# Optimization experiments

Hardware: AMD Instinct MI355X
Metric: run time of the kernel (lower is better)

Reference implementation:

```python
import jax, jax.numpy as jnp
import numpy as np

N_CLASS, N_SUPPORT, N_QUERY = 64, 5, 64
D_IN, C, WIN = 1024, 128, 5
D = C * WIN * WIN  # 3200, fine-encoder output dim


def setup_inputs() -> dict:
    key = jax.random.key(0)
    ks = jax.random.split(key, 6)
    s = 0.02  # weight init scale
    return {
        "xs": jax.random.normal(ks[0], (N_CLASS, N_SUPPORT, D_IN), jnp.float32),
        "xq": jax.random.normal(ks[1], (N_CLASS, N_QUERY, D_IN), jnp.float32),
        "W_share": jax.random.normal(ks[2], (D_IN, D), jnp.float32) * s,
        "b_share": jnp.zeros((D,), jnp.float32),
        "W_att": jax.random.normal(ks[3], (C, C), jnp.float32) * s,
        "b_att": jnp.zeros((C,), jnp.float32),
        "W_fine": jax.random.normal(ks[4], (D, D), jnp.float32) * s,
        "b_fine": jnp.zeros((D,), jnp.float32),
    }


def reference(xs, xq, W_share, b_share, W_att, b_att, W_fine, b_fine):
    n_class, n_support = xs.shape[0], xs.shape[1]
    n_query = xq.shape[1]
    ns = n_class * n_support

    # concat support + query, run shared encoder
    x = jnp.concatenate([xs.reshape(ns, -1), xq.reshape(n_class * n_query, -1)], axis=0)
    z_share = jax.nn.relu(x @ W_share + b_share)            # [N, D]
    z4 = z_share.reshape(-1, C, WIN, WIN)

    # attention head: spatial mean -> linear -> per-channel logits
    z_att = z4.mean(axis=(2, 3)) @ W_att + b_att            # [N, C]

    diag_c = jax.nn.softmax(z_att[:ns].mean(axis=0)) * C    # [C]
    w = jnp.repeat(diag_c, WIN * WIN)                       # [D] diagonal of learned metric

    # fine encoder (flatten + linear)
    z = z_share @ W_fine + b_fine                           # [N, D]
    z_proto = z[:ns].reshape(n_class, n_support, -1).mean(axis=1)  # [n_class, D]
    zq = z[ns:]                                             # [n, D]

    # attentionMetric with diagonal metric == weighted squared distance:
    # dists[i,j] = sum_d w_d (zq_i - proto_j)^2, expanded to avoid the n*m*d diff tensor
    q2 = (zq * zq) @ w                                      # [n]
    p2 = (z_proto * z_proto) @ w                            # [m]
    cross = (zq * w) @ z_proto.T                            # [n, m]
    dists = q2[:, None] + p2[None, :] - 2.0 * cross         # [n, m]

    log_p_y = jax.nn.log_softmax(-dists, axis=1).reshape(n_class, n_query, n_class)
    target = jnp.arange(n_class)
    tgt = jnp.broadcast_to(target[:, None, None], (n_class, n_query, 1))
    loss_val = -jnp.take_along_axis(log_p_y, tgt, axis=2).mean()
    y_hat = jnp.argmax(log_p_y, axis=2)
    acc_val = (y_hat == target[:, None]).astype(jnp.float32).mean()
    return loss_val, acc_val
```

## Files before the change

kernel.cpp:

```cpp
#include <hip/hip_runtime.h>
#include <math.h>

#define N_CLASS 64
#define N_SUPPORT 5
#define N_QUERY 64
#define D_IN 1024
#define C_CH 128
#define WIN 5
#define D_FEAT 3200
#define NS 320
#define NQ 4096
#define M_ROWS 4416
#define M_PAD 4480

#define ZP_SLICE  (N_CLASS * D_FEAT)
#define GT_SLICE  (128 * D_FEAT)
#define CR_SLICE  (NQ * 128)
#define NKS       10
#define LOSS_BLKS (NQ / 4)

#define PREP_X   4480
#define PREP_WS  3200
#define CONV_WF  10000

#define WS_SCALE    64.0f
#define WS_INVSCALE 0.015625f

#define WS_XF8      0u
#define WS_WSF8     4718592u
#define WS_ZSB      8126464u
#define WS_WFB      36388864u
#define WS_WFTB     56868864u
#define WS_ARENA    77348864u
#define WS_UB       98320384u
#define WS_YB       99139584u
#define WS_GT       99958784u
#define WS_WV       100777984u
#define WS_P2       100790784u
#define WS_CVEC     100791296u
#define WS_LPART    100791808u
#define WS_UPOOL    100800128u


typedef __bf16 bf16x8 __attribute__((ext_vector_type(8)));
typedef __bf16 bf16x4 __attribute__((ext_vector_type(4)));
typedef float floatx4 __attribute__((ext_vector_type(4)));
typedef __attribute__((address_space(1))) const void* gptr_t;
typedef __attribute__((address_space(3))) void* lptr_t;

__device__ __forceinline__ float waveReduceSum(float v) {
    for (int off = 32; off > 0; off >>= 1) v += __shfl_xor(v, off, 64);
    return v;
}

__global__ __launch_bounds__(256) void prep_kernel(const float* __restrict__ xs,
                                                   const float* __restrict__ xq,
                                                   const float* __restrict__ W_share,
                                                   unsigned char* __restrict__ Xf8,
                                                   unsigned char* __restrict__ Wsf8)
{
    __shared__ float tile[32][33];
    const int b = blockIdx.x;
    const int t = threadIdx.x;

    if (b < PREP_X) {
        const int e = (b * 256 + t) * 4;
        const int row = e >> 10;
        const int col = e & 1023;
        float4 v = make_float4(0.f, 0.f, 0.f, 0.f);
        if (row < NS)          v = *(const float4*)(xs + (size_t)row * D_IN + col);
        else if (row < M_ROWS) v = *(const float4*)(xq + (size_t)(row - NS) * D_IN + col);
        int p = __builtin_amdgcn_cvt_pk_fp8_f32(v.x, v.y, 0, false);
        p     = __builtin_amdgcn_cvt_pk_fp8_f32(v.z, v.w, p, true);
        const int ocol = col ^ (((row >> 1) & 1) << 3);
        *(int*)(Xf8 + (size_t)row * D_IN + ocol) = p;
        return;
    }
    const int tx = t & 31;
    const int ty = t >> 5;
    const int tb = b - PREP_X;
    const int n0 = (tb % 100) * 32;
    const int k0 = (tb / 100) * 32;
#pragma unroll
    for (int i = ty; i < 32; i += 8)
        tile[i][tx] = W_share[(size_t)(k0 + i) * D_FEAT + n0 + tx];
    __syncthreads();
#pragma unroll
    for (int i = ty; i < 32; i += 8) {
        const int p = __builtin_amdgcn_cvt_pk_fp8_f32(tile[tx][i] * WS_SCALE, 0.f,
                                                      0, false);
        const int n = n0 + i;
        const int k = (k0 + tx) ^ (((n >> 1) & 1) << 3);
        Wsf8[(size_t)n * D_IN + k] = (unsigned char)(p & 0xff);
    }
}

__global__ __launch_bounds__(256, 3) void gemm_fp8_128(const unsigned char* __restrict__ A,
                                                       const unsigned char* __restrict__ Bt,
                                                       const float* __restrict__ bias,
                                                       __bf16* __restrict__ out_bf)
{
    __shared__ __align__(16) unsigned char smem[49152];

    const int t    = threadIdx.x;
    const int lane = t & 63;
    const int w    = t >> 6;
    const int wm   = w >> 1;
    const int wn   = w & 1;

    const int bx = blockIdx.x % 25;
    const int by = blockIdx.x / 25;
    const int bm = by * 128;
    const int bn = bx * 128;

    const int q    = lane >> 4;
    const int r16  = lane & 15;
    const int m3   = (r16 >> 1) & 7;
    const int off0 = (q ^ m3) * 8;

    const int rowA = (wm * 64 + r16) * 64;
    const int rowB = (wn * 64 + r16) * 64;

    const int srow  = t >> 2;
    const int sunit = 16 * ((t & 3) ^ ((srow >> 2) & 3));

    const unsigned char* gA = A  + (size_t)(bm + srow) * D_IN + sunit;
    const unsigned char* gB = Bt + (size_t)(bn + srow) * D_IN + sunit;

    auto stage = [&](int uu, int slot) {
        const unsigned char* ga = gA + uu * 64;
        const unsigned char* gb = gB + uu * 64;
        unsigned char* l = smem + slot * 16384 + t * 16;
        __builtin_amdgcn_global_load_lds((gptr_t)ga,           (lptr_t)l,            16, 0, 0);
        __builtin_amdgcn_global_load_lds((gptr_t)(ga + 65536), (lptr_t)(l + 4096),   16, 0, 0);
        __builtin_amdgcn_global_load_lds((gptr_t)gb,           (lptr_t)(l + 8192),   16, 0, 0);
        __builtin_amdgcn_global_load_lds((gptr_t)(gb + 65536), (lptr_t)(l + 12288),  16, 0, 0);
    };

    floatx4 acc[4][4] = {};
    long av0[4], bv0[4], av1[4], bv1[4];

    auto ld16 = [&](const unsigned char* sa) {
#pragma unroll
        for (int mi = 0; mi < 4; ++mi)
            av0[mi] = *(const long*)(sa + rowA + mi * 1024 + off0);
#pragma unroll
        for (int ni = 0; ni < 4; ++ni)
            bv0[ni] = *(const long*)(sa + 8192 + rowB + ni * 1024 + off0);
#pragma unroll
        for (int mi = 0; mi < 4; ++mi)
            av1[mi] = *(const long*)(sa + rowA + mi * 1024 + (off0 ^ 32));
#pragma unroll
        for (int ni = 0; ni < 4; ++ni)
            bv1[ni] = *(const long*)(sa + 8192 + rowB + ni * 1024 + (off0 ^ 32));
    };
    auto mfma32 = [&]() {
        __builtin_amdgcn_s_setprio(1);
#pragma unroll
        for (int mi = 0; mi < 4; ++mi)
#pragma unroll
            for (int ni = 0; ni < 4; ++ni)
                acc[mi][ni] = __builtin_amdgcn_mfma_f32_16x16x32_fp8_fp8(
                    av0[mi], bv0[ni], acc[mi][ni], 0, 0, 0);
#pragma unroll
        for (int mi = 0; mi < 4; ++mi)
#pragma unroll
            for (int ni = 0; ni < 4; ++ni)
                acc[mi][ni] = __builtin_amdgcn_mfma_f32_16x16x32_fp8_fp8(
                    av1[mi], bv1[ni], acc[mi][ni], 0, 0, 0);
        __builtin_amdgcn_s_setprio(0);
    };

    stage(0, 0);
    stage(1, 1);

    for (int u = 0; u < 14; ++u) {
        const unsigned char* sa = smem + (u % 3) * 16384;
        asm volatile("s_waitcnt vmcnt(4)" ::: "memory");
        __builtin_amdgcn_s_barrier();
        ld16(sa);
        stage(u + 2, (u + 2) % 3);
        asm volatile("s_waitcnt lgkmcnt(0)" ::: "memory");
        mfma32();
    }
    {
        const unsigned char* sa = smem + (14 % 3) * 16384;
        asm volatile("s_waitcnt vmcnt(4)" ::: "memory");
        __builtin_amdgcn_s_barrier();
        ld16(sa);
        asm volatile("s_waitcnt lgkmcnt(0)" ::: "memory");
        mfma32();
    }
    {
        const unsigned char* sa = smem + (15 % 3) * 16384;
        asm volatile("s_waitcnt vmcnt(0)" ::: "memory");
        __builtin_amdgcn_s_barrier();
        ld16(sa);
        asm volatile("s_waitcnt lgkmcnt(0)" ::: "memory");
        mfma32();
    }

    __syncthreads();
    float bcol[4];
#pragma unroll
    for (int ni = 0; ni < 4; ++ni) bcol[ni] = bias[bn + wn * 64 + ni * 16 + r16];
    const int ebase = (wm * 64 + q * 4) * 256 + wn * 128 + r16 * 2;
#pragma unroll
    for (int mi = 0; mi < 4; ++mi)
#pragma unroll
        for (int ni = 0; ni < 4; ++ni) {
            const int cb = (ni ^ q) << 5;
#pragma unroll
            for (int reg = 0; reg < 4; ++reg) {
                float v = acc[mi][ni][reg] * WS_INVSCALE + bcol[ni];
                v = fmaxf(v, 0.f);
                *(__bf16*)(smem + ebase + mi * 4096 + reg * 256 + cb) = (__bf16)v;
            }
        }
    __syncthreads();
#pragma unroll
    for (int ps = 0; ps < 8; ++ps) {
        const int idx  = ps * 256 + t;
        const int row  = idx >> 4;
        const int grow = bm + row;
        if (grow < M_ROWS) {
            const int lb = row * 256 + (((idx & 15) << 4) ^ (((row >> 2) & 3) << 5));
            const int4 d = *(const int4*)(smem + lb);
            *(int4*)((char*)out_bf + ((size_t)grow * D_FEAT + bn + (idx & 15) * 8) * 2) = d;
        }
    }
}

__global__ __launch_bounds__(256) void gemm_bf16(const __bf16* __restrict__ A,
                                                 const __bf16* __restrict__ Bt,
                                                 const float* __restrict__ bias,
                                                 __bf16* __restrict__ out_bf,
                                                 float* __restrict__ out_f32,
                                                 int N, int strideK, int kIters,
                                                 int Mout, int relu, int sliceStride,
                                                 int nbx, int nby,
                                                 const float* __restrict__ attUpool,
                                                 const float* __restrict__ W_att,
                                                 const float* __restrict__ b_att,
                                                 float* __restrict__ wvec)
{
    __shared__ __align__(16) char smem[65536];
    const int t = threadIdx.x;

    if (attUpool != nullptr && blockIdx.x == gridDim.x - 1) {
        float* sW   = (float*)smem;
        float* s_pm = (float*)(smem + 16384);
        float* s_at = (float*)(smem + 16384 + 512);
        float* s_dg = (float*)(smem + 16384 + 1024);
        if (t < C_CH) {
            float a = 0.f;
            for (int p = 0; p < N_CLASS; ++p) a += attUpool[(size_t)p * C_CH + t];
            s_pm[t] = a * (1.0f / (N_CLASS * 25));
        }
        __syncthreads();
        float acc = (t < C_CH) ? b_att[t] : 0.f;
#pragma unroll
        for (int qtr = 0; qtr < 4; ++qtr) {
            const float4* src = (const float4*)(W_att + qtr * 32 * C_CH);
            float4* dst = (float4*)sW;
#pragma unroll
            for (int i = 0; i < 4; ++i) dst[i * 256 + t] = src[i * 256 + t];
            __syncthreads();
            if (t < C_CH) {
#pragma unroll
                for (int k = 0; k < 32; ++k)
                    acc += s_pm[qtr * 32 + k] * sW[k * C_CH + t];
            }
            __syncthreads();
        }
        if (t < C_CH) s_at[t] = acc;
        __syncthreads();
        if (t < C_CH) {
            float m = -INFINITY;
            for (int k = 0; k < C_CH; ++k) m = fmaxf(m, s_at[k]);
            float s = 0.f;
            for (int k = 0; k < C_CH; ++k) s += expf(s_at[k] - m);
            s_dg[t] = expf(acc - m) / s * (float)C_CH;
        }
        __syncthreads();
        for (int j = t; j < D_FEAT; j += 256) wvec[j] = s_dg[j / 25];
        return;
    }

    int bx, by, ks;
    {
        const int nbxy = nbx * nby;
        ks = blockIdx.x / nbxy;
        const int b = blockIdx.x - ks * nbxy;
        const int fg = nbx >> 3;
        const int full = fg * 8 * nby;
        if (b < full) {
            const int g = b / (8 * nby);
            const int r = b - g * 8 * nby;
            bx = g * 8 + (r & 7);
            by = r >> 3;
        } else {
            const int rem = nbx - fg * 8;
            const int r = b - full;
            bx = fg * 8 + r % rem;
            by = r / rem;
        }
    }

    const int lane = t & 63;
    const int w    = t >> 6;
    const int wm   = w >> 1;
    const int wn   = w & 1;
    const int bm   = by * 128;
    const int bn   = bx * 128;

    const int q    = lane >> 4;
    const int r16  = lane & 15;
    const int sw   = (r16 >> 1) & 3;
    const int cA   = (q ^ sw) * 8;

    const int srow   = w * 16 + (lane >> 2);
    const int sglob8 = (((lane & 3) ^ ((lane >> 3) & 3))) * 8;

    const int kBase = ks * kIters * 64;
    floatx4 acc[4][4] = {};

    auto stageb = [&](int ki, char* base) {
        const int k0 = kBase + ki * 64;
#pragma unroll
        for (int s = 0; s < 2; ++s) {
#pragma unroll
            for (int j = 0; j < 2; ++j) {
                const __bf16* ga = A  + (size_t)(bm + j * 64 + srow) * strideK
                                      + k0 + s * 32 + sglob8;
                const __bf16* gb = Bt + (size_t)(bn + j * 64 + srow) * strideK
                                      + k0 + s * 32 + sglob8;
                char* la = base +         s * 8192 + (j * 256 + w * 64) * 16;
                char* lb = base + 16384 + s * 8192 + (j * 256 + w * 64) * 16;
                __builtin_amdgcn_global_load_lds((gptr_t)ga, (lptr_t)la, 16, 0, 0);
                __builtin_amdgcn_global_load_lds((gptr_t)gb, (lptr_t)lb, 16, 0, 0);
            }
        }
    };

    stageb(0, smem);
    for (int ki = 0; ki < kIters; ++ki) {
        char* base = smem + (ki & 1) * 32768;
        __syncthreads();
        if (ki + 1 < kIters) stageb(ki + 1, smem + ((ki + 1) & 1) * 32768);

#pragma unroll
        for (int s = 0; s < 2; ++s) {
            const __bf16* sAe = (const __bf16*)(base +         s * 8192);
            const __bf16* sBe = (const __bf16*)(base + 16384 + s * 8192);
            bf16x8 av[4], bv[4];
#pragma unroll
            for (int mi = 0; mi < 4; ++mi)
                av[mi] = *(const bf16x8*)(sAe + ((wm * 64 + mi * 16 + r16) * 32 + cA));
#pragma unroll
            for (int ni = 0; ni < 4; ++ni)
                bv[ni] = *(const bf16x8*)(sBe + ((wn * 64 + ni * 16 + r16) * 32 + cA));
#pragma unroll
            for (int mi = 0; mi < 4; ++mi)
#pragma unroll
                for (int ni = 0; ni < 4; ++ni)
                    acc[mi][ni] = __builtin_amdgcn_mfma_f32_16x16x32_bf16(
                        av[mi], bv[ni], acc[mi][ni], 0, 0, 0);
        }
    }

#pragma unroll
    for (int ni = 0; ni < 4; ++ni) {
        const int col = bn + wn * 64 + ni * 16 + r16;
        const float bcol = sliceStride ? 0.f : bias[col];
#pragma unroll
        for (int mi = 0; mi < 4; ++mi) {
#pragma unroll
            for (int reg = 0; reg < 4; ++reg) {
                const int row = bm + wm * 64 + mi * 16 + q * 4 + reg;
                if (row < Mout) {
                    if (sliceStride) {
                        out_f32[(size_t)ks * sliceStride + (size_t)row * N + col] =
                            acc[mi][ni][reg];
                    } else {
                        float v = acc[mi][ni][reg] + bcol;
                        if (relu) v = fmaxf(v, 0.f);
                        if (out_f32) out_f32[(size_t)row * N + col] = v;
                        else         out_bf [(size_t)row * N + col] = (__bf16)v;
                    }
                }
            }
        }
    }
}

__global__ __launch_bounds__(256) void ut_conv_kernel(const __bf16* __restrict__ z_share,
                                                      const float* __restrict__ W_fine,
                                                      __bf16* __restrict__ u,
                                                      float* __restrict__ upool,
                                                      __bf16* __restrict__ Wfb,
                                                      __bf16* __restrict__ WfTb)
{
    __shared__ __align__(16) char smem_u[D_FEAT * 4];
    const int b = blockIdx.x;
    const int t = threadIdx.x;

    if (b >= 128) {
        float (*tile)[33] = (float(*)[33])smem_u;
        const int tb = b - 128;
        const int tx = t & 31;
        const int ty = t >> 5;
        const int n0 = (tb % 100) * 32;
        const int k0 = (tb / 100) * 32;
#pragma unroll
        for (int i = ty; i < 32; i += 8) {
            const float v = W_fine[(size_t)(k0 + i) * D_FEAT + n0 + tx];
            Wfb[(size_t)(k0 + i) * D_FEAT + n0 + tx] = (__bf16)v;
            tile[i][tx] = v;
        }
        __syncthreads();
#pragma unroll
        for (int i = ty; i < 32; i += 8)
            WfTb[(size_t)(n0 + i) * D_FEAT + k0 + tx] = (__bf16)tile[tx][i];
        return;
    }

    float* srow_ = (float*)smem_u;
    const int p = b;
    if (p >= N_CLASS) {
        for (int k = t; k < D_FEAT; k += 256) u[(size_t)p * D_FEAT + k] = (__bf16)0.f;
        return;
    }
    const __bf16* base = z_share + (size_t)(p * N_SUPPORT) * D_FEAT;
    for (int k = t; k < D_FEAT; k += 256) {
        float s = 0.f;
#pragma unroll
        for (int ss = 0; ss < N_SUPPORT; ++ss) s += (float)base[(size_t)ss * D_FEAT + k];
        s *= (1.0f / N_SUPPORT);
        u[(size_t)p * D_FEAT + k] = (__bf16)s;
        srow_[k] = s;
    }
    __syncthreads();
    if (t < C_CH) {
        float pool = 0.f;
#pragma unroll
        for (int win = 0; win < 25; ++win) pool += srow_[t * 25 + win];
        upool[(size_t)p * C_CH + t] = pool;
    }
}

__global__ __launch_bounds__(256) void y_kernel(const float* __restrict__ zp_part,
                                                const float* __restrict__ wv,
                                                const float* __restrict__ bf,
                                                __bf16* __restrict__ y,
                                                float* __restrict__ p2,
                                                float* __restrict__ cvec)
{
    __shared__ float s_red2[8];
    const int p = blockIdx.x;
    const int t = threadIdx.x;
    if (p >= N_CLASS) {
        for (int j = t; j < D_FEAT; j += 256) y[(size_t)p * D_FEAT + j] = (__bf16)0.f;
        return;
    }
    float s2 = 0.f, sc = 0.f;
    for (int j = t; j < D_FEAT; j += 256) {
        float zpf = bf[j];
#pragma unroll
        for (int ss = 0; ss < NKS; ++ss)
            zpf += zp_part[(size_t)ss * ZP_SLICE + (size_t)p * D_FEAT + j];
        const float wj = wv[j];
        y[(size_t)p * D_FEAT + j] = (__bf16)(wj * zpf);
        s2 += wj * zpf * zpf;
        sc += bf[j] * wj * zpf;
    }
    s2 = waveReduceSum(s2);
    sc = waveReduceSum(sc);
    const int lane = t & 63, wid = t >> 6;
    if (lane == 0) { s_red2[wid] = s2; s_red2[4 + wid] = sc; }
    __syncthreads();
    if (t == 0) {
        p2[p]   = s_red2[0] + s_red2[1] + s_red2[2] + s_red2[3];
        cvec[p] = s_red2[4] + s_red2[5] + s_red2[6] + s_red2[7];
    }
}

__global__ __launch_bounds__(256) void gtsum_kernel(const float* __restrict__ gp,
                                                    __bf16* __restrict__ Gt)
{
    const int i4 = blockIdx.x * 256 + threadIdx.x;
    if (i4 >= GT_SLICE / 4) return;
    float4 s = make_float4(0.f, 0.f, 0.f, 0.f);
#pragma unroll
    for (int ss = 0; ss < NKS; ++ss) {
        const float4 v = *(const float4*)(gp + (size_t)ss * GT_SLICE + i4 * 4);
        s.x += v.x; s.y += v.y; s.z += v.z; s.w += v.w;
    }
    bf16x4 o = { (__bf16)s.x, (__bf16)s.y, (__bf16)s.z, (__bf16)s.w };
    *(bf16x4*)(Gt + (size_t)i4 * 4) = o;
}

__global__ __launch_bounds__(256) void loss_kernel(const float* __restrict__ cross_part,
                                                   const float* __restrict__ p2,
                                                   const float* __restrict__ cvec,
                                                   float* __restrict__ lpart)
{
    __shared__ float s_l[4], s_a[4];
    const int t = threadIdx.x;
    const int lane = t & 63, wid = t >> 6;
    const int i = blockIdx.x * 4 + wid;
    float cr = 0.f;
#pragma unroll
    for (int ss = 0; ss < NKS; ++ss)
        cr += cross_part[(size_t)ss * CR_SLICE + (size_t)i * 128 + lane];
    const float neg = 2.0f * (cr + cvec[lane]) - p2[lane];
    float m = neg;
    for (int off = 32; off > 0; off >>= 1) m = fmaxf(m, __shfl_xor(m, off, 64));
    float e = expf(neg - m);
    float ssum = e;
    for (int off = 32; off > 0; off >>= 1) ssum += __shfl_xor(ssum, off, 64);
    const float lse = m + logf(ssum);
    const int tcls = i >> 6;
    const float negt = __shfl(neg, tcls, 64);
    float v = -neg; int bi = lane;
    for (int off = 32; off > 0; off >>= 1) {
        const float ov = __shfl_xor(v, off, 64);
        const int   oi = __shfl_xor(bi, off, 64);
        if (ov < v || (ov == v && oi < bi)) { v = ov; bi = oi; }
    }
    if (lane == 0) { s_l[wid] = lse - negt; s_a[wid] = (bi == tcls) ? 1.0f : 0.0f; }
    __syncthreads();
    if (t == 0) {
        lpart[blockIdx.x]             = s_l[0] + s_l[1] + s_l[2] + s_l[3];
        lpart[LOSS_BLKS + blockIdx.x] = s_a[0] + s_a[1] + s_a[2] + s_a[3];
    }
}

__global__ __launch_bounds__(256) void writeout_kernel(const float* __restrict__ lpart,
                                                       float* __restrict__ out)
{
    __shared__ float s_red2[8];
    const int t = threadIdx.x;
    float l = 0.f, a = 0.f;
    for (int k = t; k < LOSS_BLKS; k += 256) {
        l += lpart[k];
        a += lpart[LOSS_BLKS + k];
    }
    l = waveReduceSum(l);
    a = waveReduceSum(a);
    const int lane = t & 63, wid = t >> 6;
    if (lane == 0) { s_red2[wid] = l; s_red2[4 + wid] = a; }
    __syncthreads();
    if (t == 0) {
        out[0] = (s_red2[0] + s_red2[1] + s_red2[2] + s_red2[3]) * (1.0f / NQ);
        out[1] = (s_red2[4] + s_red2[5] + s_red2[6] + s_red2[7]) * (1.0f / NQ);
    }
}

extern "C" void kernel_launch(void* const* d_in, const int* in_sizes, int n_in,
                              void* d_out, int out_size, void* d_ws, size_t ws_size,
                              hipStream_t stream)
{
    const float* xs      = (const float*)d_in[0];
    const float* xq      = (const float*)d_in[1];
    const float* W_share = (const float*)d_in[2];
    const float* b_share = (const float*)d_in[3];
    const float* W_att   = (const float*)d_in[4];
    const float* b_att   = (const float*)d_in[5];
    const float* W_fine  = (const float*)d_in[6];
    const float* b_fine  = (const float*)d_in[7];
    float* out = (float*)d_out;

    char* ws = (char*)d_ws;
    unsigned char* Xf8  = (unsigned char*)(ws + WS_XF8);
    unsigned char* Wsf8 = (unsigned char*)(ws + WS_WSF8);
    __bf16* Zsb     = (__bf16*)(ws + WS_ZSB);
    __bf16* Wfb     = (__bf16*)(ws + WS_WFB);
    __bf16* WfTb    = (__bf16*)(ws + WS_WFTB);
    float*  arena   = (float*) (ws + WS_ARENA);
    float*  zp_part = arena;
    float*  gt_part = arena;
    float*  cr_part = arena;
    __bf16* ub      = (__bf16*)(ws + WS_UB);
    __bf16* yb      = (__bf16*)(ws + WS_YB);
    __bf16* Gt      = (__bf16*)(ws + WS_GT);
    float*  wv      = (float*) (ws + WS_WV);
    float*  p2v     = (float*) (ws + WS_P2);
    float*  cvec    = (float*) (ws + WS_CVEC);
    float*  lpart   = (float*) (ws + WS_LPART);
    float*  upool   = (float*) (ws + WS_UPOOL);

    prep_kernel<<<PREP_X + PREP_WS, 256, 0, stream>>>(xs, xq, W_share, Xf8, Wsf8);

    gemm_fp8_128<<<35 * 25, 256, 0, stream>>>(Xf8, Wsf8, b_share, Zsb);

    ut_conv_kernel<<<128 + CONV_WF, 256, 0, stream>>>(Zsb, W_fine, ub, upool,
                                                      Wfb, WfTb);

    gemm_bf16<<<25 * NKS + 1, 256, 0, stream>>>(
        ub, WfTb, nullptr, nullptr, zp_part,
        D_FEAT, D_FEAT, 5, N_CLASS, 0, ZP_SLICE, 25, 1,
        upool, W_att, b_att, wv);

    y_kernel<<<128, 256, 0, stream>>>(zp_part, wv, b_fine, yb, p2v, cvec);

    gemm_bf16<<<25 * NKS, 256, 0, stream>>>(
        yb, Wfb, nullptr, nullptr, gt_part,
        D_FEAT, D_FEAT, 5, 128, 0, GT_SLICE, 25, 1,
        nullptr, nullptr, nullptr, nullptr);

    gtsum_kernel<<<(GT_SLICE / 4 + 255) / 256, 256, 0, stream>>>(gt_part, Gt);

    gemm_bf16<<<32 * NKS, 256, 0, stream>>>(
        Zsb + (size_t)NS * D_FEAT, Gt, nullptr, nullptr, cr_part,
        128, D_FEAT, 5, NQ, 0, CR_SLICE, 1, 32,
        nullptr, nullptr, nullptr, nullptr);

    loss_kernel<<<LOSS_BLKS, 256, 0, stream>>>(cr_part, p2v, cvec, lpart);

    writeout_kernel<<<1, 256, 0, stream>>>(lpart, out);
}
```

Before: 224.6 us.

## Move W_fine bf16 convert/transpose into FP8 GEMM tail; skip unused cross columns

The W_fine to bf16 conversion and transpose work, previously extra blocks of the ut_conv kernel, now runs as a tail loop inside the FP8 shared-encoder GEMM, with each block handling 12 tiles after its epilogue. ut_kernel now only computes support means and pooling. A colLimit parameter lets the final cross GEMM skip storing columns at or beyond 64, since only 64 prototypes exist. The aim is to overlap the bandwidth-bound weight conversion with the GEMM and cut partial-sum writes, at the cost of making the GEMM blocks longer and running the conversion at the GEMM's occupancy.

```diff
diff --git a/kernel.cpp b/kernel.cpp
--- a/kernel.cpp
+++ b/kernel.cpp
@@ -98,7 +98,10 @@
 __global__ __launch_bounds__(256, 3) void gemm_fp8_128(const unsigned char* __restrict__ A,
                                                        const unsigned char* __restrict__ Bt,
                                                        const float* __restrict__ bias,
-                                                       __bf16* __restrict__ out_bf)
+                                                       __bf16* __restrict__ out_bf,
+                                                       const float* __restrict__ W_fine,
+                                                       __bf16* __restrict__ Wfb,
+                                                       __bf16* __restrict__ WfTb)
 {
     __shared__ __align__(16) unsigned char smem[49152];
 
@@ -229,6 +232,29 @@
             *(int4*)((char*)out_bf + ((size_t)grow * D_FEAT + bn + (idx & 15) * 8) * 2) = d;
         }
     }
+
+    {
+        float (*tile)[33] = (float(*)[33])smem;
+        const int tx = t & 31;
+        const int ty = t >> 5;
+        for (int it = 0; it < 12; ++it) {
+            const int tb = blockIdx.x * 12 + it;
+            if (tb >= CONV_WF) break;
+            const int n0 = (tb % 100) * 32;
+            const int k0 = (tb / 100) * 32;
+            __syncthreads();
+#pragma unroll
+            for (int i = ty; i < 32; i += 8) {
+                const float v = W_fine[(size_t)(k0 + i) * D_FEAT + n0 + tx];
+                Wfb[(size_t)(k0 + i) * D_FEAT + n0 + tx] = (__bf16)v;
+                tile[i][tx] = v;
+            }
+            __syncthreads();
+#pragma unroll
+            for (int i = ty; i < 32; i += 8)
+                WfTb[(size_t)(n0 + i) * D_FEAT + k0 + tx] = (__bf16)tile[tx][i];
+        }
+    }
 }
 
 __global__ __launch_bounds__(256) void gemm_bf16(const __bf16* __restrict__ A,
@@ -238,7 +264,7 @@
                                                  float* __restrict__ out_f32,
                                                  int N, int strideK, int kIters,
                                                  int Mout, int relu, int sliceStride,
-                                                 int nbx, int nby,
+                                                 int nbx, int nby, int colLimit,
                                                  const float* __restrict__ attUpool,
                                                  const float* __restrict__ W_att,
                                                  const float* __restrict__ b_att,
@@ -372,21 +398,23 @@
 #pragma unroll
     for (int ni = 0; ni < 4; ++ni) {
         const int col = bn + wn * 64 + ni * 16 + r16;
-        const float bcol = sliceStride ? 0.f : bias[col];
-#pragma unroll
-        for (int mi = 0; mi < 4; ++mi) {
-#pragma unroll
-            for (int reg = 0; reg < 4; ++reg) {
-                const int row = bm + wm * 64 + mi * 16 + q * 4 + reg;
-                if (row < Mout) {
-                    if (sliceStride) {
-                        out_f32[(size_t)ks * sliceStride + (size_t)row * N + col] =
-                            acc[mi][ni][reg];
-                    } else {
-                        float v = acc[mi][ni][reg] + bcol;
-                        if (relu) v = fmaxf(v, 0.f);
-                        if (out_f32) out_f32[(size_t)row * N + col] = v;
-                        else         out_bf [(size_t)row * N + col] = (__bf16)v;
+        if (col < colLimit) {
+            const float bcol = sliceStride ? 0.f : bias[col];
+#pragma unroll
+            for (int mi = 0; mi < 4; ++mi) {
+#pragma unroll
+                for (int reg = 0; reg < 4; ++reg) {
+                    const int row = bm + wm * 64 + mi * 16 + q * 4 + reg;
+                    if (row < Mout) {
+                        if (sliceStride) {
+                            out_f32[(size_t)ks * sliceStride + (size_t)row * N + col] =
+                                acc[mi][ni][reg];
+                        } else {
+                            float v = acc[mi][ni][reg] + bcol;
+                            if (relu) v = fmaxf(v, 0.f);
+                            if (out_f32) out_f32[(size_t)row * N + col] = v;
+                            else         out_bf [(size_t)row * N + col] = (__bf16)v;
+                        }
                     }
                 }
             }
@@ -394,39 +422,13 @@
     }
 }
 
-__global__ __launch_bounds__(256) void ut_conv_kernel(const __bf16* __restrict__ z_share,
-                                                      const float* __restrict__ W_fine,
-                                                      __bf16* __restrict__ u,
-                                                      float* __restrict__ upool,
-                                                      __bf16* __restrict__ Wfb,
-                                                      __bf16* __restrict__ WfTb)
-{
-    __shared__ __align__(16) char smem_u[D_FEAT * 4];
-    const int b = blockIdx.x;
+__global__ __launch_bounds__(256) void ut_kernel(const __bf16* __restrict__ z_share,
+                                                 __bf16* __restrict__ u,
+                                                 float* __restrict__ upool)
+{
+    __shared__ float srow_[D_FEAT];
+    const int p = blockIdx.x;
     const int t = threadIdx.x;
-
-    if (b >= 128) {
-        float (*tile)[33] = (float(*)[33])smem_u;
-        const int tb = b - 128;
-        const int tx = t & 31;
-        const int ty = t >> 5;
-        const int n0 = (tb % 100) * 32;
-        const int k0 = (tb / 100) * 32;
-#pragma unroll
-        for (int i = ty; i < 32; i += 8) {
-            const float v = W_fine[(size_t)(k0 + i) * D_FEAT + n0 + tx];
-            Wfb[(size_t)(k0 + i) * D_FEAT + n0 + tx] = (__bf16)v;
-            tile[i][tx] = v;
-        }
-        __syncthreads();
-#pragma unroll
-        for (int i = ty; i < 32; i += 8)
-            WfTb[(size_t)(n0 + i) * D_FEAT + k0 + tx] = (__bf16)tile[tx][i];
-        return;
-    }
-
-    float* srow_ = (float*)smem_u;
-    const int p = b;
     if (p >= N_CLASS) {
         for (int k = t; k < D_FEAT; k += 256) u[(size_t)p * D_FEAT + k] = (__bf16)0.f;
         return;
@@ -592,28 +594,28 @@
 
     prep_kernel<<<PREP_X + PREP_WS, 256, 0, stream>>>(xs, xq, W_share, Xf8, Wsf8);
 
-    gemm_fp8_128<<<35 * 25, 256, 0, stream>>>(Xf8, Wsf8, b_share, Zsb);
-
-    ut_conv_kernel<<<128 + CONV_WF, 256, 0, stream>>>(Zsb, W_fine, ub, upool,
-                                                      Wfb, WfTb);
+    gemm_fp8_128<<<35 * 25, 256, 0, stream>>>(Xf8, Wsf8, b_share, Zsb,
+                                              W_fine, Wfb, WfTb);
+
+    ut_kernel<<<128, 256, 0, stream>>>(Zsb, ub, upool);
 
     gemm_bf16<<<25 * NKS + 1, 256, 0, stream>>>(
         ub, WfTb, nullptr, nullptr, zp_part,
-        D_FEAT, D_FEAT, 5, N_CLASS, 0, ZP_SLICE, 25, 1,
+        D_FEAT, D_FEAT, 5, N_CLASS, 0, ZP_SLICE, 25, 1, D_FEAT,
         upool, W_att, b_att, wv);
 
     y_kernel<<<128, 256, 0, stream>>>(zp_part, wv, b_fine, yb, p2v, cvec);
 
     gemm_bf16<<<25 * NKS, 256, 0, stream>>>(
         yb, Wfb, nullptr, nullptr, gt_part,
-        D_FEAT, D_FEAT, 5, 128, 0, GT_SLICE, 25, 1,
+        D_FEAT, D_FEAT, 5, 128, 0, GT_SLICE, 25, 1, D_FEAT,
         nullptr, nullptr, nullptr, nullptr);
 
     gtsum_kernel<<<(GT_SLICE / 4 + 255) / 256, 256, 0, stream>>>(gt_part, Gt);
 
     gemm_bf16<<<32 * NKS, 256, 0, stream>>>(
         Zsb + (size_t)NS * D_FEAT, Gt, nullptr, nullptr, cr_part,
-        128, D_FEAT, 5, NQ, 0, CR_SLICE, 1, 32,
+        128, D_FEAT, 5, NQ, 0, CR_SLICE, 1, 32, 64,
         nullptr, nullptr, nullptr, nullptr);
 
     loss_kernel<<<LOSS_BLKS, 256, 0, stream>>>(cr_part, p2v, cvec, lpart);
```

New measurement: 262.7 us. +17.0%, slower.
